# Performance work log

Measured on AMD Instinct MI355X. Metric: run time of the kernel, lower is better.

The kernel has to match this reference:

```python
import jax, jax.numpy as jnp
import numpy as np
from jax import lax

# Shapes / module constants
B, N = 16, 1048576          # batch, events per sample (multiple of S)
H, W = 256, 256             # sensor resolution (init dim)
S = 32                      # temporal segments (hardcoded in forward)
START = 2                   # self.startIdx
SEG = N // S                # events per segment


def setup_inputs() -> dict:
    key = jax.random.key(0)
    k1, k2 = jax.random.split(key)
    xs = jax.random.randint(k1, (B, N), 0, W, dtype=jnp.int32)
    ys = jax.random.randint(k2, (B, N), 0, H, dtype=jnp.int32)
    # self.blurFilterKernel: center 0.5, surround 0.0625 (shared across groups)
    blur_kernel = jnp.array(
        [0.0625, 0.0625, 0.0625, 0.0625, 0.5, 0.0625, 0.0625, 0.0625, 0.0625],
        dtype=jnp.float32).reshape(3, 3)
    return {"xs": xs, "ys": ys, "blur_kernel": blur_kernel}


def _aligned_shift(coord, dimlen, blur_kernel):
    """Per-segment histogram along one spatial axis -> clamp -> blur -> centroid
    alignment. coord: [B, N] int32 in [0, dimlen). Returns [B, S] int32 shifts."""
    chunks = jnp.repeat(jnp.arange(S, dtype=jnp.int32), SEG)      # [N]
    idx = coord + dimlen * chunks[None, :]                         # [B, N]
    hist = jax.vmap(
        lambda i: jnp.zeros(S * dimlen, jnp.int32).at[i].add(1))(idx)
    hist = hist.astype(jnp.float32)                                # [B, S*dimlen]
    mean = hist.mean(axis=-1, keepdims=True)
    std = jnp.std(hist, axis=-1, ddof=1, keepdims=True)            # torch unbiased std
    hist = jnp.clip(hist, 0.0, mean + 3.0 * std)
    img = hist.reshape(B, 1, S, dimlen)
    # grouped conv with identical kernel per group == single-channel conv
    blurred = lax.conv_general_dilated(
        img, blur_kernel.reshape(1, 1, 3, 3), (1, 1), ((1, 1), (1, 1)))
    blurred = blurred.reshape(B, S, dimlen)
    m = jnp.einsum('bsw,w->bs', blurred,
                   jnp.arange(dimlen, dtype=jnp.float32)) / float(SEG)
    start = m[:, START:START + 1]
    # aligned = m - start - (dimlen//2 - start)
    aligned = jnp.round(m - start - (dimlen // 2 - start)).astype(jnp.int32)
    return aligned


def _accumulate(idx_c, idx_v):
    """Adaptive accumulation for one batch element.
    idx_c: [S, SEG] container indices, idx_v: [S, SEG] verifier indices."""
    container = jnp.zeros(W * H, jnp.int32).at[idx_c[START]].add(1)
    verifier = jnp.zeros((W // 2) * (H // 2), bool).at[idx_v[START]].set(True)

    def step(carry, seg):
        cont, ver, active = carry
        ic, iv = seg
        v_new = ver.at[iv].set(True)
        new_cnt = v_new.sum().astype(jnp.float32)
        xor_cnt = jnp.logical_xor(v_new, ver).sum().astype(jnp.float32)
        # original breaks when new_info ratio < 0.01 (segment NOT added)
        proceed = active & (xor_cnt / new_cnt >= 0.01)
        cont = jnp.where(proceed, cont.at[ic].add(1), cont)
        ver = jnp.where(proceed, v_new, ver)
        return (cont, ver, proceed), None

    (container, _, _), _ = lax.scan(
        step, (container, verifier, jnp.bool_(True)),
        (idx_c[START + 1:], idx_v[START + 1:]))
    return container


def _forward(xs, ys, blur_kernel):
    alignedX = _aligned_shift(xs, W, blur_kernel)   # [B, S]
    alignedY = _aligned_shift(ys, H, blur_kernel)   # [B, S]
    shX = jnp.repeat(alignedX, SEG, axis=1)          # [B, N]
    shY = jnp.repeat(alignedY, SEG, axis=1)
    xsft = jnp.clip(xs - shX, 0, W - 1)
    ysft = jnp.clip(ys - shY, 0, H - 1)
    idx_c = (xsft + W * ysft).reshape(B, S, SEG)
    idx_v = (xsft // 2 + (W // 2) * (ysft // 2)).reshape(B, S, SEG)
    containers = jax.vmap(_accumulate)(idx_c, idx_v)  # [B, W*H]
    return containers.reshape(B, 1, H, W).astype(jnp.float32)


def reference(xs, ys, blur_kernel):
    return _forward(xs, ys, blur_kernel)
```

## Files before the change

### kernel.cpp

```cpp
#include <hip/hip_runtime.h>
#include <cstdint>
#include <cstddef>

#define BB 16
#define NTOT 1048576
#define SS 32
#define SEG 32768
#define DIM 256
#define VW 512

#define OFF_PHX  0u
#define OFF_PHY  2097152u
#define OFF_BM0  0u
#define OFF_STG  1048576u
#define OFF_AX   4194304u
#define OFF_AY   4196352u
#define OFF_PR   4198400u

__device__ __forceinline__ int clamp255(int v) {
    return v < 0 ? 0 : (v > 255 ? 255 : v);
}

__global__ __launch_bounds__(256) void k_hist6(const int* __restrict__ xs,
                                               const int* __restrict__ ys,
                                               uint32_t* __restrict__ phX,
                                               uint32_t* __restrict__ phY) {
    int blk = blockIdx.x;
    int p = blk & 3;
    int arr = (blk >> 2) & 1;
    int s = (blk >> 3) & 31;
    int b = blk >> 8;
    int t = threadIdx.x;
    const int* src = arr ? ys : xs;
    uint32_t* dst = arr ? phY : phX;
    __shared__ uint32_t ph[256][32];
    uint32_t* phl = (uint32_t*)ph;
#pragma unroll
    for (int i = 0; i < 32; ++i) phl[t + i * 256] = 0u;
    __syncthreads();
    int c = t & 31;
    const int4* p4 = (const int4*)(src + (size_t)b * NTOT + (size_t)s * SEG
                                   + (size_t)p * 8192);
#pragma unroll
    for (int i = 0; i < 8; ++i) {
        int4 v = p4[i * 256 + t];
        atomicAdd(&ph[v.x][c], 1u);
        atomicAdd(&ph[v.y][c], 1u);
        atomicAdd(&ph[v.z][c], 1u);
        atomicAdd(&ph[v.w][c], 1u);
    }
    __syncthreads();
    uint32_t sum = 0u;
#pragma unroll
    for (int j = 0; j < 32; ++j)
        sum += ph[t][(j + t) & 31];
    dst[((size_t)(b * SS + s) * 4 + p) * 256 + t] = sum;
}

__global__ __launch_bounds__(512) void k_shifts(const uint32_t* __restrict__ phX,
                                                const uint32_t* __restrict__ phY,
                                                const float* __restrict__ blurk,
                                                int* __restrict__ alignedX,
                                                int* __restrict__ alignedY) {
    int blk = blockIdx.x;
    int b = blk >> 1, axis = blk & 1;
    const uint32_t* hist = (axis == 0 ? phX : phY) + (size_t)b * SS * 4 * 256;
    int* out = (axis == 0 ? alignedX : alignedY) + b * SS;

    __shared__ float vals[SS][DIM];
    __shared__ double wsq[8];
    __shared__ float mrow[SS];
    int t = threadIdx.x;
    int w = t >> 6, lane = t & 63;
    int c0 = lane << 2;

    double lsq = 0.0;
    for (int r = w; r < SS; r += 8) {
        const uint32_t* hr = hist + (size_t)(r * 4) * 256 + c0;
        uint4 a0 = *(const uint4*)(hr);
        uint4 a1 = *(const uint4*)(hr + 256);
        uint4 a2 = *(const uint4*)(hr + 512);
        uint4 a3 = *(const uint4*)(hr + 768);
        uint32_t u0 = a0.x + a1.x + a2.x + a3.x;
        uint32_t u1 = a0.y + a1.y + a2.y + a3.y;
        uint32_t u2 = a0.z + a1.z + a2.z + a3.z;
        uint32_t u3 = a0.w + a1.w + a2.w + a3.w;
        float v0 = (float)u0, v1 = (float)u1, v2 = (float)u2, v3 = (float)u3;
        vals[r][c0 + 0] = v0; vals[r][c0 + 1] = v1;
        vals[r][c0 + 2] = v2; vals[r][c0 + 3] = v3;
        double d0 = (double)v0 - 128.0, d1 = (double)v1 - 128.0;
        double d2 = (double)v2 - 128.0, d3 = (double)v3 - 128.0;
        lsq += d0 * d0 + d1 * d1 + d2 * d2 + d3 * d3;
    }
    for (int o = 32; o > 0; o >>= 1) lsq += __shfl_xor(lsq, o, 64);
    if (lane == 0) wsq[w] = lsq;
    __syncthreads();
    float s2 = (float)(wsq[0] + wsq[1] + wsq[2] + wsq[3]
                     + wsq[4] + wsq[5] + wsq[6] + wsq[7]);
    float sd = sqrtf(s2 / 8191.0f);
    float thr = 128.0f + 3.0f * sd;

    float k00 = blurk[0], k01 = blurk[1], k02 = blurk[2];
    float k10 = blurk[3], k11 = blurk[4], k12 = blurk[5];
    float k20 = blurk[6], k21 = blurk[7], k22 = blurk[8];

#define V(r, c) fminf(vals[r][c], thr)
    for (int s = w; s < SS; s += 8) {
        double dot = 0.0;
#pragma unroll
        for (int j = 0; j < 4; ++j) {
            int c = c0 + j;
            int cm = c - 1, cp = c + 1;
            bool cml = (cm >= 0), cpl = (cp < DIM);
            float bsum = 0.0f;
            if (s - 1 >= 0) {
                if (cml) bsum += k00 * V(s - 1, cm);
                bsum += k01 * V(s - 1, c);
                if (cpl) bsum += k02 * V(s - 1, cp);
            }
            if (cml) bsum += k10 * V(s, cm);
            bsum += k11 * V(s, c);
            if (cpl) bsum += k12 * V(s, cp);
            if (s + 1 < SS) {
                if (cml) bsum += k20 * V(s + 1, cm);
                bsum += k21 * V(s + 1, c);
                if (cpl) bsum += k22 * V(s + 1, cp);
            }
            dot += (double)bsum * (double)c;
        }
        for (int o = 32; o > 0; o >>= 1) dot += __shfl_xor(dot, o, 64);
        if (lane == 0) mrow[s] = (float)(dot / 32768.0);
    }
#undef V
    __syncthreads();

    if (t < SS) {
        float start = mrow[2];
        float a = mrow[t] - start;
        float c = 128.0f - start;
        out[t] = (int)rintf(a - c);
    }
}

__global__ __launch_bounds__(256) void k_bitmap_g(const int* __restrict__ xs,
                                                  const int* __restrict__ ys,
                                                  const int* __restrict__ aX,
                                                  const int* __restrict__ aY,
                                                  uint32_t* __restrict__ bmp,
                                                  uint32_t* __restrict__ staging) {
    int blk = blockIdx.x;
    int p = blk & 1;
    int sl = (blk >> 1) & 7;
    int b = blk >> 4;
    int t = threadIdx.x;
    {
        uint32_t* stg = staging + (size_t)blk * 2048;
#pragma unroll
        for (int i = 0; i < 8; ++i) stg[t + i * 256] = 0u;
    }
    int s = 2 + sl;
    int shx = aX[b * SS + s];
    int shy = aY[b * SS + s];
    __shared__ uint32_t bm[VW];
    bm[t] = 0u; bm[t + 256] = 0u;
    __syncthreads();
    size_t base = (size_t)b * NTOT + (size_t)s * SEG + (size_t)p * (SEG / 2);
    const int4* x4 = (const int4*)(xs + base);
    const int4* y4 = (const int4*)(ys + base);
    for (int i = 0; i < 16; ++i) {
        int4 xv = x4[i * 256 + t];
        int4 yv = y4[i * 256 + t];
#define DOV(xc, yc) { int xf = clamp255((xc) - shx); int yf = clamp255((yc) - shy); \
                      int iv = (xf >> 1) + ((yf >> 1) << 7); \
                      atomicOr(&bm[iv >> 5], 1u << (iv & 31)); }
        DOV(xv.x, yv.x) DOV(xv.y, yv.y) DOV(xv.z, yv.z) DOV(xv.w, yv.w)
#undef DOV
    }
    __syncthreads();
    uint32_t* outp = bmp + ((size_t)(b * 8 + sl) * 2 + p) * VW;
    outp[t] = bm[t];
    outp[t + 256] = bm[t + 256];
}

__global__ __launch_bounds__(256) void k_scan_tail(const int* __restrict__ xs,
                                                   const int* __restrict__ ys,
                                                   const int* __restrict__ aX,
                                                   const int* __restrict__ aY,
                                                   const uint32_t* __restrict__ bmp,
                                                   int* __restrict__ proceed) {
    int b = blockIdx.x;
    int t = threadIdx.x;
    __shared__ uint32_t ver[VW];
    __shared__ uint32_t bm[VW];
    __shared__ int wred[4];
    __shared__ int sh_flag;
    __shared__ int sh_total;

    for (int i = t; i < 30; i += 256) proceed[b * SS + 2 + i] = 0;
    int active = 1;
    const uint32_t* base = bmp + (size_t)b * 8 * 2 * VW;
    int wid = t >> 6, lane = t & 63;

    {
        uint32_t w0 = base[t] | base[VW + t];
        uint32_t w1 = base[t + 256] | base[VW + t + 256];
        ver[t] = w0; ver[t + 256] = w1;
        int c = __popc(w0) + __popc(w1);
        for (int o = 32; o > 0; o >>= 1) c += __shfl_down(c, o, 64);
        if (lane == 0) wred[wid] = c;
        __syncthreads();
        if (t == 0) {
            sh_total = wred[0] + wred[1] + wred[2] + wred[3];
            proceed[b * SS + 2] = 1;
        }
    }
    __syncthreads();

    for (int sl = 1; sl < 8; ++sl) {
        uint32_t w0 = base[(size_t)(sl * 2) * VW + t]
                    | base[(size_t)(sl * 2 + 1) * VW + t];
        uint32_t w1 = base[(size_t)(sl * 2) * VW + t + 256]
                    | base[(size_t)(sl * 2 + 1) * VW + t + 256];
        int c = __popc(w0 & ~ver[t]) + __popc(w1 & ~ver[t + 256]);
        for (int o = 32; o > 0; o >>= 1) c += __shfl_down(c, o, 64);
        if (lane == 0) wred[wid] = c;
        __syncthreads();
        if (t == 0) {
            int newly = wred[0] + wred[1] + wred[2] + wred[3];
            int total = sh_total + newly;
            float ratio = (float)newly / (float)total;
            int f = (ratio >= 0.01f) ? 1 : 0;
            sh_flag = f;
            if (f) {
                sh_total = total;
                proceed[b * SS + 2 + sl] = 1;
            }
        }
        __syncthreads();
        if (!sh_flag) { active = 0; break; }
        ver[t] |= w0;
        ver[t + 256] |= w1;
        __syncthreads();
    }
    if (!active) return;

    for (int s = 10; s < SS; ++s) {
        int shx = aX[b * SS + s];
        int shy = aY[b * SS + s];
        bm[t] = 0u; bm[t + 256] = 0u;
        __syncthreads();
        const int4* x4 = (const int4*)(xs + (size_t)b * NTOT + (size_t)s * SEG);
        const int4* y4 = (const int4*)(ys + (size_t)b * NTOT + (size_t)s * SEG);
        for (int i = 0; i < 32; ++i) {
            int4 xv = x4[i * 256 + t];
            int4 yv = y4[i * 256 + t];
#define DOV(xc, yc) { int xf = clamp255((xc) - shx); int yf = clamp255((yc) - shy); \
                      int iv = (xf >> 1) + ((yf >> 1) << 7); \
                      atomicOr(&bm[iv >> 5], 1u << (iv & 31)); }
            DOV(xv.x, yv.x) DOV(xv.y, yv.y) DOV(xv.z, yv.z) DOV(xv.w, yv.w)
#undef DOV
        }
        __syncthreads();
        uint32_t w0 = bm[t], w1 = bm[t + 256];
        int c = __popc(w0 & ~ver[t]) + __popc(w1 & ~ver[t + 256]);
        for (int o = 32; o > 0; o >>= 1) c += __shfl_down(c, o, 64);
        if (lane == 0) wred[wid] = c;
        __syncthreads();
        if (t == 0) {
            int newly = wred[0] + wred[1] + wred[2] + wred[3];
            int total = sh_total + newly;
            float ratio = (float)newly / (float)total;
            int f = (ratio >= 0.01f) ? 1 : 0;
            sh_flag = f;
            if (f) {
                sh_total = total;
                proceed[b * SS + s] = 1;
            }
        }
        __syncthreads();
        if (!sh_flag) break;
        ver[t] |= w0;
        ver[t + 256] |= w1;
        __syncthreads();
    }
}

__global__ __launch_bounds__(1024) void k_accum7(const int* __restrict__ xs,
                                                 const int* __restrict__ ys,
                                                 const int* __restrict__ aX,
                                                 const int* __restrict__ aY,
                                                 const int* __restrict__ proceed,
                                                 uint32_t* __restrict__ staging) {
    int blk = blockIdx.x;
    int p = blk & 7, half = (blk >> 3) & 1, b = blk >> 4;
    __shared__ uint32_t acc[16384];
    int t = threadIdx.x;
    for (int i = t; i < 16384; i += 1024) acc[i] = 0u;
    __syncthreads();
    int ybase = half << 7;
    for (int s = 2; s < SS; ++s) {
        if (!proceed[b * SS + s]) continue;
        int shx = aX[b * SS + s];
        int shy = aY[b * SS + s];
        size_t base = (size_t)b * NTOT + (size_t)s * SEG + (size_t)p * 4096;
        int4 xv = ((const int4*)(xs + base))[t];
        int4 yv = ((const int4*)(ys + base))[t];
#define DOC(xc, yc) { int xf = clamp255((xc) - shx); int yf = clamp255((yc) - shy); \
                      if ((yf >> 7) == half) { \
                          int cell = xf + ((yf - ybase) << 8); \
                          atomicAdd(&acc[cell >> 1], 1u << ((cell & 1) << 4)); } }
        DOC(xv.x, yv.x) DOC(xv.y, yv.y) DOC(xv.z, yv.z) DOC(xv.w, yv.w)
#undef DOC
    }
    __syncthreads();
    uint32_t* stg = staging + (size_t)b * 32768 + ((size_t)half << 14);
    for (int i = t; i < 16384; i += 1024) {
        uint32_t w = acc[i];
        if (w) atomicAdd(&stg[i], w);
    }
}

__global__ __launch_bounds__(1024) void k_convert(const uint32_t* __restrict__ staging,
                                                  float* __restrict__ out) {
    int g = blockIdx.x * 1024 + threadIdx.x;
    uint32_t w = staging[g];
    ((float2*)out)[g] = make_float2((float)(w & 0xFFFFu), (float)(w >> 16));
}

extern "C" void kernel_launch(void* const* d_in, const int* in_sizes, int n_in,
                              void* d_out, int out_size, void* d_ws, size_t ws_size,
                              hipStream_t stream) {
    const int* xs = (const int*)d_in[0];
    const int* ys = (const int*)d_in[1];
    const float* blurk = (const float*)d_in[2];
    float* out = (float*)d_out;

    uint8_t* ws = (uint8_t*)d_ws;
    uint32_t* phX = (uint32_t*)(ws + OFF_PHX);
    uint32_t* phY = (uint32_t*)(ws + OFF_PHY);
    int* aX = (int*)(ws + OFF_AX);
    int* aY = (int*)(ws + OFF_AY);
    int* proceed = (int*)(ws + OFF_PR);
    uint32_t* bm0 = (uint32_t*)(ws + OFF_BM0);
    uint32_t* staging = (uint32_t*)(ws + OFF_STG);

    k_hist6<<<BB * SS * 2 * 4, 256, 0, stream>>>(xs, ys, phX, phY);
    k_shifts<<<BB * 2, 512, 0, stream>>>(phX, phY, blurk, aX, aY);
    k_bitmap_g<<<BB * 8 * 2, 256, 0, stream>>>(xs, ys, aX, aY, bm0, staging);
    k_scan_tail<<<BB, 256, 0, stream>>>(xs, ys, aX, aY, bm0, proceed);
    k_accum7<<<BB * 2 * 8, 1024, 0, stream>>>(xs, ys, aX, aY, proceed, staging);
    k_convert<<<512, 1024, 0, stream>>>(staging, out);
}
```

Measured before the change: 67.15 us.

## Fuse bitmap and scan kernels via last-block-done counter; move staging zeroing

Merges the per-segment bitmap kernel and the per-batch scan kernel into one launch. Each batch's 16 blocks publish their bitmaps, bump an atomic counter, and the last block to finish runs the sequential scan. Zeroing of the staging buffer moves into the histogram kernel, and the workspace layout is moved so the regions no longer alias. This removes one kernel launch and its gap, at the cost of threadfence and atomic overhead plus a larger workspace.

```diff
diff --git a/kernel.cpp b/kernel.cpp
--- a/kernel.cpp
+++ b/kernel.cpp
@@ -11,11 +11,12 @@
 
 #define OFF_PHX  0u
 #define OFF_PHY  2097152u
-#define OFF_BM0  0u
-#define OFF_STG  1048576u
-#define OFF_AX   4194304u
-#define OFF_AY   4196352u
-#define OFF_PR   4198400u
+#define OFF_BM0  4194304u
+#define OFF_STG  5242880u
+#define OFF_AX   7340032u
+#define OFF_AY   7342080u
+#define OFF_PR   7344128u
+#define OFF_DONE 7346176u
 
 __device__ __forceinline__ int clamp255(int v) {
     return v < 0 ? 0 : (v > 255 ? 255 : v);
@@ -24,13 +25,18 @@
 __global__ __launch_bounds__(256) void k_hist6(const int* __restrict__ xs,
                                                const int* __restrict__ ys,
                                                uint32_t* __restrict__ phX,
-                                               uint32_t* __restrict__ phY) {
+                                               uint32_t* __restrict__ phY,
+                                               uint32_t* __restrict__ staging,
+                                               int* __restrict__ done) {
     int blk = blockIdx.x;
     int p = blk & 3;
     int arr = (blk >> 2) & 1;
     int s = (blk >> 3) & 31;
     int b = blk >> 8;
     int t = threadIdx.x;
+    if (t < 128) staging[(size_t)blk * 128 + t] = 0u;
+    if (blk == 0 && t < 16) done[t] = 0;
+
     const int* src = arr ? ys : xs;
     uint32_t* dst = arr ? phY : phX;
     __shared__ uint32_t ph[256][32];
@@ -142,65 +148,58 @@
     }
 }
 
-__global__ __launch_bounds__(256) void k_bitmap_g(const int* __restrict__ xs,
-                                                  const int* __restrict__ ys,
-                                                  const int* __restrict__ aX,
-                                                  const int* __restrict__ aY,
-                                                  uint32_t* __restrict__ bmp,
-                                                  uint32_t* __restrict__ staging) {
+__global__ __launch_bounds__(256) void k_bitmap_scan(const int* __restrict__ xs,
+                                                     const int* __restrict__ ys,
+                                                     const int* __restrict__ aX,
+                                                     const int* __restrict__ aY,
+                                                     uint32_t* __restrict__ bmp,
+                                                     int* __restrict__ proceed,
+                                                     int* __restrict__ done) {
     int blk = blockIdx.x;
     int p = blk & 1;
     int sl = (blk >> 1) & 7;
     int b = blk >> 4;
     int t = threadIdx.x;
-    {
-        uint32_t* stg = staging + (size_t)blk * 2048;
-#pragma unroll
-        for (int i = 0; i < 8; ++i) stg[t + i * 256] = 0u;
-    }
     int s = 2 + sl;
     int shx = aX[b * SS + s];
     int shy = aY[b * SS + s];
     __shared__ uint32_t bm[VW];
+    __shared__ uint32_t ver[VW];
+    __shared__ int wred[4];
+    __shared__ int sh_flag;
+    __shared__ int sh_total;
+    __shared__ int sh_rank;
     bm[t] = 0u; bm[t + 256] = 0u;
     __syncthreads();
-    size_t base = (size_t)b * NTOT + (size_t)s * SEG + (size_t)p * (SEG / 2);
-    const int4* x4 = (const int4*)(xs + base);
-    const int4* y4 = (const int4*)(ys + base);
-    for (int i = 0; i < 16; ++i) {
-        int4 xv = x4[i * 256 + t];
-        int4 yv = y4[i * 256 + t];
+    size_t base_el = (size_t)b * NTOT + (size_t)s * SEG + (size_t)p * (SEG / 2);
+    {
+        const int4* x4 = (const int4*)(xs + base_el);
+        const int4* y4 = (const int4*)(ys + base_el);
+        for (int i = 0; i < 16; ++i) {
+            int4 xv = x4[i * 256 + t];
+            int4 yv = y4[i * 256 + t];
 #define DOV(xc, yc) { int xf = clamp255((xc) - shx); int yf = clamp255((yc) - shy); \
                       int iv = (xf >> 1) + ((yf >> 1) << 7); \
                       atomicOr(&bm[iv >> 5], 1u << (iv & 31)); }
-        DOV(xv.x, yv.x) DOV(xv.y, yv.y) DOV(xv.z, yv.z) DOV(xv.w, yv.w)
+            DOV(xv.x, yv.x) DOV(xv.y, yv.y) DOV(xv.z, yv.z) DOV(xv.w, yv.w)
 #undef DOV
+        }
     }
     __syncthreads();
     uint32_t* outp = bmp + ((size_t)(b * 8 + sl) * 2 + p) * VW;
     outp[t] = bm[t];
     outp[t + 256] = bm[t + 256];
-}
-
-__global__ __launch_bounds__(256) void k_scan_tail(const int* __restrict__ xs,
-                                                   const int* __restrict__ ys,
-                                                   const int* __restrict__ aX,
-                                                   const int* __restrict__ aY,
-                                                   const uint32_t* __restrict__ bmp,
-                                                   int* __restrict__ proceed) {
-    int b = blockIdx.x;
-    int t = threadIdx.x;
-    __shared__ uint32_t ver[VW];
-    __shared__ uint32_t bm[VW];
-    __shared__ int wred[4];
-    __shared__ int sh_flag;
-    __shared__ int sh_total;
+    __threadfence();
+    __syncthreads();
+    if (t == 0) sh_rank = atomicAdd(&done[b], 1);
+    __syncthreads();
+    if (sh_rank != 15) return;
+    __threadfence();
 
     for (int i = t; i < 30; i += 256) proceed[b * SS + 2 + i] = 0;
     int active = 1;
     const uint32_t* base = bmp + (size_t)b * 8 * 2 * VW;
     int wid = t >> 6, lane = t & 63;
-
     {
         uint32_t w0 = base[t] | base[VW + t];
         uint32_t w1 = base[t + 256] | base[VW + t + 256];
@@ -215,12 +214,11 @@
         }
     }
     __syncthreads();
-
-    for (int sl = 1; sl < 8; ++sl) {
-        uint32_t w0 = base[(size_t)(sl * 2) * VW + t]
-                    | base[(size_t)(sl * 2 + 1) * VW + t];
-        uint32_t w1 = base[(size_t)(sl * 2) * VW + t + 256]
-                    | base[(size_t)(sl * 2 + 1) * VW + t + 256];
+    for (int sl2 = 1; sl2 < 8; ++sl2) {
+        uint32_t w0 = base[(size_t)(sl2 * 2) * VW + t]
+                    | base[(size_t)(sl2 * 2 + 1) * VW + t];
+        uint32_t w1 = base[(size_t)(sl2 * 2) * VW + t + 256]
+                    | base[(size_t)(sl2 * 2 + 1) * VW + t + 256];
         int c = __popc(w0 & ~ver[t]) + __popc(w1 & ~ver[t + 256]);
         for (int o = 32; o > 0; o >>= 1) c += __shfl_down(c, o, 64);
         if (lane == 0) wred[wid] = c;
@@ -233,7 +231,7 @@
             sh_flag = f;
             if (f) {
                 sh_total = total;
-                proceed[b * SS + 2 + sl] = 1;
+                proceed[b * SS + 2 + sl2] = 1;
             }
         }
         __syncthreads();
@@ -244,17 +242,17 @@
     }
     if (!active) return;
 
-    for (int s = 10; s < SS; ++s) {
-        int shx = aX[b * SS + s];
-        int shy = aY[b * SS + s];
+    for (int s2 = 10; s2 < SS; ++s2) {
+        int shx2 = aX[b * SS + s2];
+        int shy2 = aY[b * SS + s2];
         bm[t] = 0u; bm[t + 256] = 0u;
         __syncthreads();
-        const int4* x4 = (const int4*)(xs + (size_t)b * NTOT + (size_t)s * SEG);
-        const int4* y4 = (const int4*)(ys + (size_t)b * NTOT + (size_t)s * SEG);
+        const int4* x4 = (const int4*)(xs + (size_t)b * NTOT + (size_t)s2 * SEG);
+        const int4* y4 = (const int4*)(ys + (size_t)b * NTOT + (size_t)s2 * SEG);
         for (int i = 0; i < 32; ++i) {
             int4 xv = x4[i * 256 + t];
             int4 yv = y4[i * 256 + t];
-#define DOV(xc, yc) { int xf = clamp255((xc) - shx); int yf = clamp255((yc) - shy); \
+#define DOV(xc, yc) { int xf = clamp255((xc) - shx2); int yf = clamp255((yc) - shy2); \
                       int iv = (xf >> 1) + ((yf >> 1) << 7); \
                       atomicOr(&bm[iv >> 5], 1u << (iv & 31)); }
             DOV(xv.x, yv.x) DOV(xv.y, yv.y) DOV(xv.z, yv.z) DOV(xv.w, yv.w)
@@ -274,7 +272,7 @@
             sh_flag = f;
             if (f) {
                 sh_total = total;
-                proceed[b * SS + s] = 1;
+                proceed[b * SS + s2] = 1;
             }
         }
         __syncthreads();
@@ -341,13 +339,13 @@
     int* aX = (int*)(ws + OFF_AX);
     int* aY = (int*)(ws + OFF_AY);
     int* proceed = (int*)(ws + OFF_PR);
+    int* done = (int*)(ws + OFF_DONE);
     uint32_t* bm0 = (uint32_t*)(ws + OFF_BM0);
     uint32_t* staging = (uint32_t*)(ws + OFF_STG);
 
-    k_hist6<<<BB * SS * 2 * 4, 256, 0, stream>>>(xs, ys, phX, phY);
+    k_hist6<<<BB * SS * 2 * 4, 256, 0, stream>>>(xs, ys, phX, phY, staging, done);
     k_shifts<<<BB * 2, 512, 0, stream>>>(phX, phY, blurk, aX, aY);
-    k_bitmap_g<<<BB * 8 * 2, 256, 0, stream>>>(xs, ys, aX, aY, bm0, staging);
-    k_scan_tail<<<BB, 256, 0, stream>>>(xs, ys, aX, aY, bm0, proceed);
+    k_bitmap_scan<<<BB * 8 * 2, 256, 0, stream>>>(xs, ys, aX, aY, bm0, proceed, done);
     k_accum7<<<BB * 2 * 8, 1024, 0, stream>>>(xs, ys, aX, aY, proceed, staging);
     k_convert<<<512, 1024, 0, stream>>>(staging, out);
 }
```

Measured after the change: 86.26 us. 1.28x slower.
